# Kernel tuning notes

Measured on AMD Instinct MI355X. Metric: run time of the kernel, lower is better.

Reference implementation:

```python
import jax, jax.numpy as jnp
import numpy as np

P = 256          # patch_num (number of patches / batches)
PT = 64          # point_num per patch (hard-coded in source)
N = P * PT       # total input points
D = 768          # feature dim
R2 = 0.3 ** 2    # radius^2 for neighbor search
K = 9            # max_num_neighbors


def _new_points():
    # voxgrid [-0.2,0.2,4] x [-0.2,0.2,4], z = 0 -> (16,3), matches torch meshgrid/view
    x = np.linspace(-0.2, 0.2, 4)
    xy = np.stack(np.meshgrid(x, x)).reshape(2, -1).T        # (16, 2)
    return jnp.asarray(np.concatenate([xy, np.zeros((16, 1))], axis=1), jnp.float32)


def setup_inputs() -> dict:
    key = jax.random.key(0)
    ks = jax.random.split(key, 16)
    lin = lambda k, i, o: jax.random.normal(k, (i, o), jnp.float32) / np.sqrt(i)
    vec = lambda o: jnp.zeros((o,), jnp.float32)
    return dict(
        x=jax.random.normal(ks[0], (N, D), jnp.float32),
        pos=jax.random.uniform(ks[1], (N, 3), jnp.float32),
        batch=jnp.repeat(jnp.arange(P, dtype=jnp.int32), PT),
        diff=jax.random.normal(ks[2], (N, 3), jnp.float32),
        local_fea=jax.random.normal(ks[3], (P, D), jnp.float32),
        sw1=lin(ks[4], D + 3, 256), sb1=vec(256),
        sw2=lin(ks[5], 256, 128), sb2=vec(128),
        sw3=lin(ks[6], 128, 3), sb3=vec(3),
        cw1=lin(ks[7], 6, 64), cb1=vec(64),
        cw2=lin(ks[8], 64, 128), cb2=vec(128),
        mw1=lin(ks[9], D + 128, 512), mb1=vec(512),
        mw2=lin(ks[10], 512, 256), mb2=vec(256),
        mw3=lin(ks[11], 256, 9), mb3=vec(9),
    )


def reference(x, pos, batch, diff, local_fea, sw1, sb1, sw2, sb2, sw3, sb3,
              cw1, cb1, cw2, cb2, mw1, mb1, mw2, mb2, mw3, mb3):
    relu = jax.nn.relu
    # broadcast patch-level feature to points: repeat_interleave -> (N, 768)
    lf = jnp.repeat(local_fea.reshape(P, D), PT, axis=0)
    # shift MLP (source MLP applies ReLU after EVERY layer, incl. the last), then tanh
    h = relu(jnp.concatenate([lf, pos], -1) @ sw1 + sb1)
    h = relu(h @ sw2 + sb2)
    h = relu(h @ sw3 + sb3)
    n_pos = jnp.tanh(h) + pos                                   # (N, 3)
    pos_c = jnp.concatenate([pos, n_pos], axis=0)               # (2N, 3)
    # per-patch radius graph: patch b owns its 64 original + 64 shifted points
    pp = jnp.concatenate([pos.reshape(P, PT, 3), n_pos.reshape(P, PT, 3)], axis=1)  # (P,128,3)
    d2 = jnp.sum((pp[:, :, None, :] - pp[:, None, :, :]) ** 2, -1)                  # (P,128,128)
    d2 = jnp.where(d2 <= R2, d2, jnp.inf)
    neg_d, idx = jax.lax.top_k(-d2, K)          # up to K nearest within radius (self incl.)
    ok = jnp.isfinite(neg_d)                    # (P,128,K) valid-slot mask
    nbr = pp[jnp.arange(P)[:, None, None], idx]                 # gather: (P,128,K,3)
    rel = nbr - pp[:, :, None, :]
    feat = jnp.concatenate([nbr, rel], -1)      # PointConv message: [x_j, pos_j - pos_i]
    m = relu(feat @ cw1 + cb1)
    m = relu(m @ cw2 + cb2)                                     # (P,128,K,128)
    m = jnp.where(ok[..., None], m, -jnp.inf)
    agg = jnp.max(m, axis=2)                                    # max-aggregate -> (P,128,128)
    # restore concat(pos, n_pos) row ordering of pos_c
    pos_fea = jnp.concatenate([agg[:, :PT].reshape(N, 128), agg[:, PT:].reshape(N, 128)], axis=0)
    rot_fea = jnp.concatenate([jnp.concatenate([lf, lf], 0), pos_fea], -1)  # (2N, 896)
    g = relu(rot_fea @ mw1 + mb1)
    g = relu(g @ mw2 + mb2)
    g = relu(g @ mw3 + mb3)                                     # (2N, 9)
    rot = g.reshape(-1, 3, 3)                                   # (2N,3,3)
    rot_constrain = jnp.einsum('nki,nkj->nij', rot, rot)        # R^T @ R
    npts = _new_points()                                        # (16,3)
    # repeat_interleave(rot,16) bmm tiled grid: row k uses rot[k//16], point[k%16]
    delta = jnp.einsum('nij,tj->nti', rot, npts).reshape(-1, 3)  # (32N,3)
    M = 2 * N
    # source uses pos_c.view(M,3,1).repeat(16,1,1): center for row k is pos_c[k % M]
    center = pos_c[jnp.arange(16 * M) % M]
    plane_init = (delta + center).reshape(P, -1, 3)             # (P, 2048, 3)
    return plane_init, rot_constrain
```

## Files before the change

kernel.cpp:

```cpp
#include <hip/hip_runtime.h>


#define P 256
#define PT 64
#define NPTS 16384
#define M2N 32768
#define D 768
#define SENTK 0xFFFFFFFFFFFFFFFFull

typedef __attribute__((ext_vector_type(8))) short bfrag;
typedef __attribute__((ext_vector_type(4))) float ffrag;

#define MFMA16(a, b, c) __builtin_amdgcn_mfma_f32_16x16x32_bf16((a), (b), (c), 0, 0, 0)

__device__ __forceinline__ ushort f2bf(float x) {
  unsigned u = __float_as_uint(x);
  u = (u + 0x7FFFu + ((u >> 16) & 1u)) >> 16;
  return (ushort)u;
}
__device__ __forceinline__ float bf2f(ushort u) {
  return __uint_as_float((unsigned)u << 16);
}

__global__ __launch_bounds__(256) void patch_pre2(
    const float* __restrict__ lf, const float* __restrict__ sw1,
    const float* __restrict__ sb1, const float* __restrict__ mw1,
    const float* __restrict__ mb1, double* __restrict__ A1d, float* __restrict__ B1) {
  __shared__ float lfs[768];
  const int b = blockIdx.x, t = threadIdx.x;
  const int p = b / 3, chunk = b % 3;
  for (int i = t; i < 768; i += 256) lfs[i] = lf[p * 768 + i];
  __syncthreads();
  if (chunk == 0) {
    double a = (double)sb1[t];
    for (int d = 0; d < 768; ++d)
      a += (double)lfs[d] * (double)sw1[d * 256 + t];
    A1d[p * 256 + t] = a;
  } else {
    const int c = (chunk - 1) * 256 + t;
    float bb = 0.f;
    for (int d = 0; d < 768; ++d)
      bb += lfs[d] * mw1[d * 512 + c];
    B1[p * 512 + c] = mb1[c] + bb;
  }
}

__global__ __launch_bounds__(512, 4) void point_mlp6(
    const float* __restrict__ pos, const float* __restrict__ sw1,
    const float* __restrict__ sw2, const float* __restrict__ sb2,
    const float* __restrict__ sw3, const float* __restrict__ sb3,
    const double* __restrict__ A1d, double* __restrict__ ppd, float* __restrict__ ppf) {
  __shared__ double smemD[8704];
  __shared__ double posd[96];
  double* h1T = smemD;
  double* h2s = smemD;

  const int b = blockIdx.x, t = threadIdx.x;
  const int p = b >> 1, qb = b & 1;
  if (t < 96) posd[t] = (double)pos[p * 192 + qb * 96 + t];
  __syncthreads();

  {
    const int k = t & 255, rb = (t >> 8) * 16;
    const double a1 = A1d[p * 256 + k];
    const double w0 = (double)sw1[768 * 256 + k];
    const double w1 = (double)sw1[769 * 256 + k];
    const double w2 = (double)sw1[770 * 256 + k];
    for (int r = rb; r < rb + 16; ++r) {
      const double* pp = &posd[r * 3];
      const double v = a1 + pp[0] * w0 + pp[1] * w1 + pp[2] * w2;
      h1T[k * 34 + r] = v > 0.0 ? v : 0.0;
    }
  }
  __syncthreads();

  {
    const int c = t & 127, ptq = t >> 7;
    double acc[8];
    #pragma unroll
    for (int i = 0; i < 8; ++i) acc[i] = 0.0;
    const float* wp = sw2 + c;
    const double* hp = h1T + ptq * 8;
    #pragma unroll 4
    for (int k = 0; k < 256; ++k) {
      const double2 h01 = *(const double2*)&hp[k * 34];
      const double2 h23 = *(const double2*)&hp[k * 34 + 2];
      const double2 h45 = *(const double2*)&hp[k * 34 + 4];
      const double2 h67 = *(const double2*)&hp[k * 34 + 6];
      const double w = (double)wp[k * 128];
      acc[0] += h01.x * w;
      acc[1] += h01.y * w;
      acc[2] += h23.x * w;
      acc[3] += h23.y * w;
      acc[4] += h45.x * w;
      acc[5] += h45.y * w;
      acc[6] += h67.x * w;
      acc[7] += h67.y * w;
    }
    __syncthreads();
    #pragma unroll
    for (int i = 0; i < 8; ++i) {
      const int pt = ptq * 8 + i;
      const double u = acc[i] + (double)sb2[c];
      h2s[pt * 129 + c] = u > 0.0 ? u : 0.0;
    }
  }
  __syncthreads();

  if (t < 96) {
    const int r = t / 3, j = t % 3;
    double u = (double)sb3[j];
    #pragma unroll 4
    for (int c = 0; c < 128; ++c)
      u += h2s[r * 129 + c] * (double)sw3[c * 3 + j];
    u = u > 0.0 ? u : 0.0;
    const int s = qb * 32 + r;
    const double po = posd[r * 3 + j];
    const double np_ = tanh(u) + po;
    const size_t rn = (size_t)(p * 128 + 64 + s) * 3 + j;
    const size_t ro = (size_t)(p * 128 + s) * 3 + j;
    ppd[rn] = np_;  ppf[rn] = (float)np_;
    ppd[ro] = po;   ppf[ro] = (float)po;
  }
}

__device__ __forceinline__ void ins9(unsigned long long* s, unsigned long long key) {
  #pragma unroll
  for (int k = 8; k >= 1; --k) {
    const unsigned long long lo = s[k - 1];
    const unsigned long long mx = key > lo ? key : lo;
    s[k] = (key >= s[k]) ? s[k] : mx;
  }
  s[0] = key < s[0] ? key : s[0];
}

__global__ __launch_bounds__(512) void neighbors_k2(const double* __restrict__ ppd,
                                                    int* __restrict__ nbr) {
  __shared__ double PX[128], PY[128], PZ[128];
  __shared__ unsigned long long mbuf[2][128][9];
  const int p = blockIdx.x, t = threadIdx.x;
  const int row = t & 127, seg = t >> 7;
  if (t < 128) {
    PX[t] = ppd[(p * 128 + t) * 3 + 0];
    PY[t] = ppd[(p * 128 + t) * 3 + 1];
    PZ[t] = ppd[(p * 128 + t) * 3 + 2];
  }
  __syncthreads();
  const double R2d = 0.3 * 0.3;
  const double xi = PX[row], yi = PY[row], zi = PZ[row];
  unsigned long long s[9];
  #pragma unroll
  for (int k = 0; k < 9; ++k) s[k] = SENTK;
  const int j0 = seg * 32;
  for (int jj = 0; jj < 32; ++jj) {
    const int j = j0 + jj;
    const double dx = PX[j] - xi, dy = PY[j] - yi, dz = PZ[j] - zi;
    const double d2 = dx * dx + dy * dy + dz * dz;
    unsigned long long key =
        (((unsigned long long)__double_as_longlong(d2)) & ~127ull) | (unsigned long long)j;
    key = (d2 <= R2d) ? key : SENTK;
    ins9(s, key);
  }
  if (seg & 1) {
    #pragma unroll
    for (int k = 0; k < 9; ++k) mbuf[seg >> 1][row][k] = s[k];
  }
  __syncthreads();
  if (!(seg & 1)) {
    #pragma unroll
    for (int m = 0; m < 9; ++m) ins9(s, mbuf[seg >> 1][row][m]);
  }
  if (seg == 2) {
    #pragma unroll
    for (int k = 0; k < 9; ++k) mbuf[1][row][k] = s[k];
  }
  __syncthreads();
  if (seg == 0) {
    #pragma unroll
    for (int m = 0; m < 9; ++m) ins9(s, mbuf[1][row][m]);
    #pragma unroll
    for (int k = 0; k < 9; ++k)
      nbr[(p * 128 + row) * 9 + k] = (s[k] == SENTK) ? -1 : (int)(s[k] & 127);
  }
}

__global__ __launch_bounds__(256) void prepack_w(
    const float* __restrict__ mw1, const float* __restrict__ mw2,
    const float* __restrict__ mw3, const float* __restrict__ cw2,
    ushort* __restrict__ W1p, ushort* __restrict__ W2p, ushort* __restrict__ W3p,
    ushort* __restrict__ C2h, ushort* __restrict__ C2l) {
  const int idx = blockIdx.x * 256 + threadIdx.x;
  if (idx < 65536) {
    const int j = idx & 7, l = (idx >> 3) & 63, kt = (idx >> 9) & 3, nt = idx >> 11;
    const int k = kt * 32 + (l >> 4) * 8 + j, n = nt * 16 + (l & 15);
    W1p[idx] = f2bf(mw1[(768 + k) * 512 + n]);
  } else if (idx < 196608) {
    const int q = idx - 65536;
    const int j = q & 7, l = (q >> 3) & 63, kt = (q >> 9) & 15, nt = q >> 13;
    const int k = kt * 32 + (l >> 4) * 8 + j, n = nt * 16 + (l & 15);
    W2p[q] = f2bf(mw2[k * 256 + n]);
  } else if (idx < 200704) {
    const int q = idx - 196608;
    const int j = q & 7, l = (q >> 3) & 63, kt = q >> 9;
    const int k = kt * 32 + (l >> 4) * 8 + j, n = l & 15;
    W3p[q] = (n < 9) ? f2bf(mw3[k * 9 + n]) : (ushort)0;
  } else if (idx < 208896) {
    const int q = idx - 200704;
    const int j = q & 7, l = (q >> 3) & 63, kt = (q >> 9) & 1, nt = q >> 10;
    const int k = kt * 32 + (l >> 4) * 8 + j, n = nt * 16 + (l & 15);
    const float v = cw2[k * 128 + n];
    const ushort hi = f2bf(v);
    C2h[q] = hi;
    C2l[q] = f2bf(v - bf2f(hi));
  }
}

#define EPITCH 80
#define M2PITCH 132
__global__ __launch_bounds__(512, 6) void edge_mfma(
    const float* __restrict__ ppf, const int* __restrict__ nbr,
    const float* __restrict__ cw1, const float* __restrict__ cb1,
    const ushort* __restrict__ C2h, const ushort* __restrict__ C2l,
    const float* __restrict__ cb2, ushort* __restrict__ aggB) {
  __shared__ float posL[128 * 3];
  __shared__ int nbrL[144];
  __shared__ __align__(16) ushort buf[2 * 144 * EPITCH];
  ushort* m1h = buf;
  ushort* m1l = buf + 144 * EPITCH;
  ushort* m2L = buf;

  const int b = blockIdx.x, t = threadIdx.x;
  const int p = b >> 3, off = (b & 7) * 16;
  for (int i = t; i < 384; i += 512) posL[i] = ppf[p * 384 + i];
  if (t < 144) nbrL[t] = nbr[(p * 128 + off) * 9 + t];
  __syncthreads();

  {
    const int c0 = (t & 31) * 2, eg = t >> 5;
    float w1a[6], w1b[6];
    #pragma unroll
    for (int q = 0; q < 6; ++q) {
      w1a[q] = cw1[q * 64 + c0];
      w1b[q] = cw1[q * 64 + c0 + 1];
    }
    const float b1a = cb1[c0], b1b = cb1[c0 + 1];
    for (int e = eg; e < 144; e += 16) {
      const int pl = e / 9;
      const int j = nbrL[e];
      const int jj = j < 0 ? 0 : j;
      const int ctr = off + pl;
      const float nx = posL[jj * 3], ny = posL[jj * 3 + 1], nz = posL[jj * 3 + 2];
      const float cx = posL[ctr * 3], cy = posL[ctr * 3 + 1], cz = posL[ctr * 3 + 2];
      float va = b1a + nx * w1a[0] + ny * w1a[1] + nz * w1a[2] +
                 (nx - cx) * w1a[3] + (ny - cy) * w1a[4] + (nz - cz) * w1a[5];
      va = fmaxf(va, 0.f);
      float vb = b1b + nx * w1b[0] + ny * w1b[1] + nz * w1b[2] +
                 (nx - cx) * w1b[3] + (ny - cy) * w1b[4] + (nz - cz) * w1b[5];
      vb = fmaxf(vb, 0.f);
      const ushort hia = f2bf(va), hib = f2bf(vb);
      const ushort loa = f2bf(va - bf2f(hia)), lob = f2bf(vb - bf2f(hib));
      *(unsigned*)&m1h[e * EPITCH + c0] = (unsigned)hia | ((unsigned)hib << 16);
      *(unsigned*)&m1l[e * EPITCH + c0] = (unsigned)loa | ((unsigned)lob << 16);
    }
  }
  __syncthreads();

  const int w = t >> 6, l = t & 63, lrow = l & 15, quad = l >> 4;
  ffrag acc[9];
  {
    bfrag Bh[2], Bl[2];
    #pragma unroll
    for (int kt = 0; kt < 2; ++kt) {
      const int bi = ((w * 2 + kt) * 64 + l) * 8;
      Bh[kt] = *(const bfrag*)&C2h[bi];
      Bl[kt] = *(const bfrag*)&C2l[bi];
    }
    #pragma unroll
    for (int mt = 0; mt < 9; ++mt) {
      bfrag Ah[2], Al[2];
      #pragma unroll
      for (int kt = 0; kt < 2; ++kt) {
        const int ai = (mt * 16 + lrow) * EPITCH + kt * 32 + quad * 8;
        Ah[kt] = *(const bfrag*)&m1h[ai];
        Al[kt] = *(const bfrag*)&m1l[ai];
      }
      ffrag a = (ffrag){0.f, 0.f, 0.f, 0.f};
      #pragma unroll
      for (int kt = 0; kt < 2; ++kt) {
        a = MFMA16(Ah[kt], Bh[kt], a);
        a = MFMA16(Ah[kt], Bl[kt], a);
        a = MFMA16(Al[kt], Bh[kt], a);
      }
      acc[mt] = a;
    }
  }
  __syncthreads();

  {
    const float cbv = cb2[w * 16 + lrow];
    const int col = w * 16 + lrow;
    #pragma unroll
    for (int mt = 0; mt < 9; ++mt) {
      #pragma unroll
      for (int r = 0; r < 4; ++r) {
        const int row = mt * 16 + quad * 4 + r;
        m2L[row * M2PITCH + col] = f2bf(fmaxf(acc[mt][r] + cbv, 0.f));
      }
    }
  }
  __syncthreads();

  for (int o = t; o < 1024; o += 512) {
    const int pt = o >> 6, cc = (o & 63) * 2;
    ushort b0 = 0, b1 = 0;
    #pragma unroll
    for (int s = 0; s < 9; ++s) {
      if (nbrL[pt * 9 + s] >= 0) {
        const unsigned u = *(const unsigned*)&m2L[(pt * 9 + s) * M2PITCH + cc];
        const ushort u0 = (ushort)u, u1 = (ushort)(u >> 16);
        b0 = u0 > b0 ? u0 : b0;
        b1 = u1 > b1 ? u1 : b1;
      }
    }
    *(unsigned*)&aggB[(size_t)(p * 128 + off + pt) * 128 + cc] =
        (unsigned)b0 | ((unsigned)b1 << 16);
  }
}

#define PA  136
#define PG1 520
#define PG2 264
__global__ __launch_bounds__(256) void final_mlp_mfma(
    const ushort* __restrict__ aggB, const float* __restrict__ B1,
    const ushort* __restrict__ W1p, const ushort* __restrict__ W2p,
    const ushort* __restrict__ W3p, const float* __restrict__ mb2,
    const float* __restrict__ mb3, float* __restrict__ rotw,
    float* __restrict__ out_rc) {
  __shared__ __align__(16) ushort g1T[32 * PG1];
  __shared__ __align__(16) ushort reg2[32 * PG2];
  __shared__ float rotL[32 * 9];
  const int b = blockIdx.x, t = threadIdx.x;
  const int w = t >> 6, l = t & 63;
  const int lrow = l & 15, quad = l >> 4;
  int p, off;
  if (b < 512) { p = b >> 1;         off = (b & 1) * 32; }
  else         { p = (b - 512) >> 1; off = 64 + ((b - 512) & 1) * 32; }
  const int n0 = b * 32;

  {
    ushort* aT = reg2;
    const int r0 = t >> 3, sg = (t & 7) * 16;
    const ushort* src = aggB + (size_t)(p * 128 + off + r0) * 128 + sg;
    const uint4 v0 = *(const uint4*)src;
    const uint4 v1 = *(const uint4*)(src + 8);
    *(uint4*)&aT[r0 * PA + sg] = v0;
    *(uint4*)&aT[r0 * PA + sg + 8] = v1;
  }
  __syncthreads();

  {
    const ushort* aT = reg2;
    bfrag a[2][4];
    #pragma unroll
    for (int mt = 0; mt < 2; ++mt)
      #pragma unroll
      for (int kt = 0; kt < 4; ++kt)
        a[mt][kt] = *(const bfrag*)&aT[(mt * 16 + lrow) * PA + kt * 32 + quad * 8];
    ffrag acc[2][8];
    #pragma unroll
    for (int nti = 0; nti < 8; ++nti) {
      const float bv = B1[p * 512 + (w * 8 + nti) * 16 + lrow];
      acc[0][nti] = (ffrag){bv, bv, bv, bv};
      acc[1][nti] = acc[0][nti];
    }
    #pragma unroll
    for (int nti = 0; nti < 8; ++nti) {
      const int nt = w * 8 + nti;
      #pragma unroll
      for (int kt = 0; kt < 4; ++kt) {
        const bfrag bb = *(const bfrag*)&W1p[((nt * 4 + kt) * 64 + l) * 8];
        acc[0][nti] = MFMA16(a[0][kt], bb, acc[0][nti]);
        acc[1][nti] = MFMA16(a[1][kt], bb, acc[1][nti]);
      }
    }
    #pragma unroll
    for (int mt = 0; mt < 2; ++mt)
      #pragma unroll
      for (int nti = 0; nti < 8; ++nti) {
        const int col = (w * 8 + nti) * 16 + lrow;
        #pragma unroll
        for (int r = 0; r < 4; ++r)
          g1T[(mt * 16 + quad * 4 + r) * PG1 + col] = f2bf(fmaxf(acc[mt][nti][r], 0.f));
      }
  }
  __syncthreads();

  {
    bfrag a[2][16];
    #pragma unroll
    for (int mt = 0; mt < 2; ++mt)
      #pragma unroll
      for (int kt = 0; kt < 16; ++kt)
        a[mt][kt] = *(const bfrag*)&g1T[(mt * 16 + lrow) * PG1 + kt * 32 + quad * 8];
    ffrag acc[2][4];
    #pragma unroll
    for (int nti = 0; nti < 4; ++nti) {
      acc[0][nti] = (ffrag){0.f, 0.f, 0.f, 0.f};
      acc[1][nti] = acc[0][nti];
    }
    #pragma unroll
    for (int nti = 0; nti < 4; ++nti) {
      const int nt = w * 4 + nti;
      #pragma unroll
      for (int kt = 0; kt < 16; ++kt) {
        const bfrag bb = *(const bfrag*)&W2p[((nt * 16 + kt) * 64 + l) * 8];
        acc[0][nti] = MFMA16(a[0][kt], bb, acc[0][nti]);
        acc[1][nti] = MFMA16(a[1][kt], bb, acc[1][nti]);
      }
    }
    ushort* g2T = reg2;
    #pragma unroll
    for (int mt = 0; mt < 2; ++mt)
      #pragma unroll
      for (int nti = 0; nti < 4; ++nti) {
        const int col = (w * 4 + nti) * 16 + lrow;
        const float bv = mb2[col];
        #pragma unroll
        for (int r = 0; r < 4; ++r)
          g2T[(mt * 16 + quad * 4 + r) * PG2 + col] =
              f2bf(fmaxf(acc[mt][nti][r] + bv, 0.f));
      }
  }
  __syncthreads();

  if (w < 2) {
    const ushort* g2T = reg2;
    ffrag acc = (ffrag){0.f, 0.f, 0.f, 0.f};
    #pragma unroll
    for (int kt = 0; kt < 8; ++kt) {
      const bfrag aa = *(const bfrag*)&g2T[(w * 16 + lrow) * PG2 + kt * 32 + quad * 8];
      const bfrag bb = *(const bfrag*)&W3p[(kt * 64 + l) * 8];
      acc = MFMA16(aa, bb, acc);
    }
    if (lrow < 9) {
      const float bv = mb3[lrow];
      #pragma unroll
      for (int r = 0; r < 4; ++r) {
        const int m = w * 16 + quad * 4 + r;
        const float u = fmaxf(acc[r] + bv, 0.f);
        rotL[m * 9 + lrow] = u;
        rotw[(size_t)(n0 + m) * 9 + lrow] = u;
      }
    }
  }
  __syncthreads();

  for (int idx = t; idx < 288; idx += 256) {
    const int r = idx / 9, e = idx % 9, ii = e / 3, jj = e % 3;
    const float* R = &rotL[r * 9];
    out_rc[(size_t)(n0 + r) * 9 + e] =
        R[ii] * R[jj] + R[3 + ii] * R[3 + jj] + R[6 + ii] * R[6 + jj];
  }
}

__global__ __launch_bounds__(256) void plane_k(const float* __restrict__ rotw,
                                               const float* __restrict__ ppf,
                                               float* __restrict__ out_plane) {
  const int q = blockIdx.x * 256 + threadIdx.x;
  const int n = q >> 4, tt = q & 15;
  const float* R = &rotw[n * 9];
  const int tx = tt & 3, ty = tt >> 2;
  const double step = 0.4 / 3.0;
  const float X = (tx == 3) ? 0.2f : (float)((double)tx * step - 0.2);
  const float Y = (ty == 3) ? 0.2f : (float)((double)ty * step - 0.2);
  const int m = q & (M2N - 1);
  int p, s;
  if (m < NPTS) { p = m >> 6; s = m & 63; }
  else          { const int mm = m - NPTS; p = mm >> 6; s = 64 + (mm & 63); }
  const float* C = &ppf[(p * 128 + s) * 3];
  #pragma unroll
  for (int i2 = 0; i2 < 3; ++i2) {
    const float d = R[i2 * 3 + 0] * X + R[i2 * 3 + 1] * Y;
    out_plane[q * 3 + i2] = d + C[i2];
  }
}

extern "C" void kernel_launch(void* const* d_in, const int* in_sizes, int n_in,
                              void* d_out, int out_size, void* d_ws, size_t ws_size,
                              hipStream_t stream) {
  const float* pos       = (const float*)d_in[1];
  const float* local_fea = (const float*)d_in[4];
  const float* sw1 = (const float*)d_in[5];
  const float* sb1 = (const float*)d_in[6];
  const float* sw2 = (const float*)d_in[7];
  const float* sb2 = (const float*)d_in[8];
  const float* sw3 = (const float*)d_in[9];
  const float* sb3 = (const float*)d_in[10];
  const float* cw1 = (const float*)d_in[11];
  const float* cb1 = (const float*)d_in[12];
  const float* cw2 = (const float*)d_in[13];
  const float* cb2 = (const float*)d_in[14];
  const float* mw1 = (const float*)d_in[15];
  const float* mb1 = (const float*)d_in[16];
  const float* mw2 = (const float*)d_in[17];
  const float* mb2 = (const float*)d_in[18];
  const float* mw3 = (const float*)d_in[19];
  const float* mb3 = (const float*)d_in[20];

  char* ws = (char*)d_ws;
  double* A1d  = (double*)(ws + 0);
  double* ppd  = (double*)(ws + 524288);
  float*  B1   = (float*)(ws + 1310720);
  float*  ppf  = (float*)(ws + 1835008);
  int*    nbr  = (int*)(ws + 2228224);
  ushort* aggB = (ushort*)(ws + 3407872);
  float*  rotw = (float*)(ws + 11796480);
  ushort* W1p  = (ushort*)(ws + 12976128);
  ushort* W2p  = (ushort*)(ws + 13107200);
  ushort* W3p  = (ushort*)(ws + 13369344);
  ushort* C2h  = (ushort*)(ws + 13377536);
  ushort* C2l  = (ushort*)(ws + 13393920);

  float* out_plane = (float*)d_out;
  float* out_rc = out_plane + 1572864;

  patch_pre2<<<768, 256, 0, stream>>>(local_fea, sw1, sb1, mw1, mb1, A1d, B1);
  point_mlp6<<<512, 512, 0, stream>>>(pos, sw1, sw2, sb2, sw3, sb3, A1d, ppd, ppf);
  neighbors_k2<<<256, 512, 0, stream>>>(ppd, nbr);
  prepack_w<<<816, 256, 0, stream>>>(mw1, mw2, mw3, cw2, W1p, W2p, W3p, C2h, C2l);
  edge_mfma<<<2048, 512, 0, stream>>>(ppf, nbr, cw1, cb1, C2h, C2l, cb2, aggB);
  final_mlp_mfma<<<1024, 256, 0, stream>>>(aggB, B1, W1p, W2p, W3p, mb2, mb3, rotw, out_rc);
  plane_k<<<2048, 256, 0, stream>>>(rotw, ppf, out_plane);
}
```

Before: 258.6 us.

## Fuse plane generation into final MLP and stage sw2 weights in LDS

The plane computation is folded into the final MLP kernel. It now reads the rotation matrices from shared memory, so the rotw global round trip and one kernel launch go away. Separately, point_mlp6 double-buffers 8-row tiles of sw2 into shared memory instead of reading the weight column directly from global inside the inner loop. That adds a barrier per tile and 8 KB of LDS, which may lower occupancy for that kernel.

```diff
diff --git a/kernel.cpp b/kernel.cpp
--- a/kernel.cpp
+++ b/kernel.cpp
@@ -52,6 +52,7 @@
     const double* __restrict__ A1d, double* __restrict__ ppd, float* __restrict__ ppf) {
   __shared__ double smemD[8704];
   __shared__ double posd[96];
+  __shared__ __align__(16) float bufW[2][1024];
   double* h1T = smemD;
   double* h2s = smemD;
 
@@ -72,6 +73,7 @@
       h1T[k * 34 + r] = v > 0.0 ? v : 0.0;
     }
   }
+  *(float2*)&bufW[0][t * 2] = *(const float2*)&sw2[t * 2];
   __syncthreads();
 
   {
@@ -79,25 +81,33 @@
     double acc[8];
     #pragma unroll
     for (int i = 0; i < 8; ++i) acc[i] = 0.0;
-    const float* wp = sw2 + c;
     const double* hp = h1T + ptq * 8;
-    #pragma unroll 4
-    for (int k = 0; k < 256; ++k) {
-      const double2 h01 = *(const double2*)&hp[k * 34];
-      const double2 h23 = *(const double2*)&hp[k * 34 + 2];
-      const double2 h45 = *(const double2*)&hp[k * 34 + 4];
-      const double2 h67 = *(const double2*)&hp[k * 34 + 6];
-      const double w = (double)wp[k * 128];
-      acc[0] += h01.x * w;
-      acc[1] += h01.y * w;
-      acc[2] += h23.x * w;
-      acc[3] += h23.y * w;
-      acc[4] += h45.x * w;
-      acc[5] += h45.y * w;
-      acc[6] += h67.x * w;
-      acc[7] += h67.y * w;
-    }
-    __syncthreads();
+    #pragma unroll 1
+    for (int kt = 0; kt < 32; ++kt) {
+      const int cur = kt & 1;
+      if (kt < 31) {
+        const float2 v = *(const float2*)&sw2[(kt + 1) * 1024 + t * 2];
+        *(float2*)&bufW[cur ^ 1][t * 2] = v;
+      }
+      #pragma unroll
+      for (int kk = 0; kk < 8; ++kk) {
+        const int k = kt * 8 + kk;
+        const double2 h01 = *(const double2*)&hp[k * 34];
+        const double2 h23 = *(const double2*)&hp[k * 34 + 2];
+        const double2 h45 = *(const double2*)&hp[k * 34 + 4];
+        const double2 h67 = *(const double2*)&hp[k * 34 + 6];
+        const double w = (double)bufW[cur][kk * 128 + c];
+        acc[0] += h01.x * w;
+        acc[1] += h01.y * w;
+        acc[2] += h23.x * w;
+        acc[3] += h23.y * w;
+        acc[4] += h45.x * w;
+        acc[5] += h45.y * w;
+        acc[6] += h67.x * w;
+        acc[7] += h67.y * w;
+      }
+      __syncthreads();
+    }
     #pragma unroll
     for (int i = 0; i < 8; ++i) {
       const int pt = ptq * 8 + i;
@@ -334,8 +344,8 @@
     const ushort* __restrict__ aggB, const float* __restrict__ B1,
     const ushort* __restrict__ W1p, const ushort* __restrict__ W2p,
     const ushort* __restrict__ W3p, const float* __restrict__ mb2,
-    const float* __restrict__ mb3, float* __restrict__ rotw,
-    float* __restrict__ out_rc) {
+    const float* __restrict__ mb3, const float* __restrict__ ppf,
+    float* __restrict__ out_plane, float* __restrict__ out_rc) {
   __shared__ __align__(16) ushort g1T[32 * PG1];
   __shared__ __align__(16) ushort reg2[32 * PG2];
   __shared__ float rotL[32 * 9];
@@ -447,9 +457,7 @@
       #pragma unroll
       for (int r = 0; r < 4; ++r) {
         const int m = w * 16 + quad * 4 + r;
-        const float u = fmaxf(acc[r] + bv, 0.f);
-        rotL[m * 9 + lrow] = u;
-        rotw[(size_t)(n0 + m) * 9 + lrow] = u;
+        rotL[m * 9 + lrow] = fmaxf(acc[r] + bv, 0.f);
       }
     }
   }
@@ -461,27 +469,25 @@
     out_rc[(size_t)(n0 + r) * 9 + e] =
         R[ii] * R[jj] + R[3 + ii] * R[3 + jj] + R[6 + ii] * R[6 + jj];
   }
-}
-
-__global__ __launch_bounds__(256) void plane_k(const float* __restrict__ rotw,
-                                               const float* __restrict__ ppf,
-                                               float* __restrict__ out_plane) {
-  const int q = blockIdx.x * 256 + threadIdx.x;
-  const int n = q >> 4, tt = q & 15;
-  const float* R = &rotw[n * 9];
-  const int tx = tt & 3, ty = tt >> 2;
-  const double step = 0.4 / 3.0;
-  const float X = (tx == 3) ? 0.2f : (float)((double)tx * step - 0.2);
-  const float Y = (ty == 3) ? 0.2f : (float)((double)ty * step - 0.2);
-  const int m = q & (M2N - 1);
-  int p, s;
-  if (m < NPTS) { p = m >> 6; s = m & 63; }
-  else          { const int mm = m - NPTS; p = mm >> 6; s = 64 + (mm & 63); }
-  const float* C = &ppf[(p * 128 + s) * 3];
-  #pragma unroll
-  for (int i2 = 0; i2 < 3; ++i2) {
-    const float d = R[i2 * 3 + 0] * X + R[i2 * 3 + 1] * Y;
-    out_plane[q * 3 + i2] = d + C[i2];
+
+  for (int ii = t; ii < 512; ii += 256) {
+    const int q = n0 * 16 + ii;
+    const int n_loc = ii >> 4, tt = ii & 15;
+    const float* R = &rotL[n_loc * 9];
+    const int tx = tt & 3, ty = tt >> 2;
+    const double step = 0.4 / 3.0;
+    const float X = (tx == 3) ? 0.2f : (float)((double)tx * step - 0.2);
+    const float Y = (ty == 3) ? 0.2f : (float)((double)ty * step - 0.2);
+    const int m = q & (M2N - 1);
+    int pp, s;
+    if (m < NPTS) { pp = m >> 6; s = m & 63; }
+    else          { const int mm = m - NPTS; pp = mm >> 6; s = 64 + (mm & 63); }
+    const float* C = &ppf[(pp * 128 + s) * 3];
+    #pragma unroll
+    for (int i2 = 0; i2 < 3; ++i2) {
+      const float d = R[i2 * 3 + 0] * X + R[i2 * 3 + 1] * Y;
+      out_plane[(size_t)q * 3 + i2] = d + C[i2];
+    }
   }
 }
 
@@ -514,7 +520,6 @@
   float*  ppf  = (float*)(ws + 1835008);
   int*    nbr  = (int*)(ws + 2228224);
   ushort* aggB = (ushort*)(ws + 3407872);
-  float*  rotw = (float*)(ws + 11796480);
   ushort* W1p  = (ushort*)(ws + 12976128);
   ushort* W2p  = (ushort*)(ws + 13107200);
   ushort* W3p  = (ushort*)(ws + 13369344);
@@ -529,6 +534,6 @@
   neighbors_k2<<<256, 512, 0, stream>>>(ppd, nbr);
   prepack_w<<<816, 256, 0, stream>>>(mw1, mw2, mw3, cw2, W1p, W2p, W3p, C2h, C2l);
   edge_mfma<<<2048, 512, 0, stream>>>(ppf, nbr, cw1, cb1, C2h, C2l, cb2, aggB);
-  final_mlp_mfma<<<1024, 256, 0, stream>>>(aggB, B1, W1p, W2p, W3p, mb2, mb3, rotw, out_rc);
-  plane_k<<<2048, 256, 0, stream>>>(rotw, ppf, out_plane);
-}
+  final_mlp_mfma<<<1024, 256, 0, stream>>>(aggB, B1, W1p, W2p, W3p, mb2, mb3,
+                                           ppf, out_plane, out_rc);
+}
```

Result: no change. 261.7 us (+1.2%).
